# Kernel optimization log

Measured on AMD Instinct MI355X. Metric: run time of the kernel, lower is better.

Reference implementation:

```python
import jax, jax.numpy as jnp
import numpy as np

# Sizes: B graphs of N nodes each, K nearest neighbours, D=feat_dim=nhid, C=pos_dim
B, N, K, D, C = 4, 1024, 128, 32, 2
L = 3                     # number of EGNN conv layers
E_IN = 2 * D + 1          # edge MLP input: feats_i | feats_j | rel_dist (edge_dim=0, fourier=0)
E_H = 2 * E_IN            # edge MLP hidden


def _lin(key, fan_in, fan_out):
    kw, kb = jax.random.split(key)
    w = jax.random.normal(kw, (fan_in, fan_out), jnp.float32) / np.sqrt(fan_in)
    b = jax.random.normal(kb, (fan_out,), jnp.float32) * 0.01
    return w, b


def _stack(key, fan_in, fan_out):
    ws, bs = zip(*[_lin(k, fan_in, fan_out) for k in jax.random.split(key, L)])
    return jnp.stack(ws), jnp.stack(bs)


def setup_inputs() -> dict:
    key = jax.random.key(0)
    ks = jax.random.split(key, 10)
    feat_ = jax.random.normal(ks[0], (B * N, D), jnp.float32)
    coor_ = jax.random.normal(ks[1], (B * N, C), jnp.float32)
    batch = jnp.full((B,), N, dtype=jnp.int32)   # per-graph node counts (equal-size graphs)
    embed_w, embed_b = _lin(ks[2], D, D)         # embed: Linear(feat_dim, nhid)
    e1_w, e1_b = _stack(ks[3], E_IN, E_H)        # edge MLP
    e2_w, e2_b = _stack(ks[4], E_H, D)           # -> m_dim = nhid
    gate_w, gate_b = _stack(ks[5], D, 1)         # soft_edges gate
    c1_w, c1_b = _stack(ks[6], D, 4 * D)         # coors MLP
    c2_w, c2_b = _stack(ks[7], 4 * D, 1)
    n1_w, n1_b = _stack(ks[8], 2 * D, 2 * D)     # node MLP
    n2_w, n2_b = _stack(ks[9], 2 * D, D)
    coors_scale = jnp.full((L, 1), 1e-2, jnp.float32)  # CoorsNorm scale (init 1e-2)
    return dict(feat_=feat_, coor_=coor_, batch=batch, embed_w=embed_w, embed_b=embed_b,
                e1_w=e1_w, e1_b=e1_b, e2_w=e2_w, e2_b=e2_b, gate_w=gate_w, gate_b=gate_b,
                c1_w=c1_w, c1_b=c1_b, c2_w=c2_w, c2_b=c2_b, n1_w=n1_w, n1_b=n1_b,
                n2_w=n2_w, n2_b=n2_b, coors_scale=coors_scale)


def _lrelu(x):
    return jax.nn.leaky_relu(x, 0.1)


def _gather(x, idx):
    # x: [B, n, d], idx: [B, n, k] -> [B, n, k, d]
    return jax.vmap(lambda xb, ib: xb[ib])(x, idx)


def _egnn_layer(feats, coors, p):
    (e1_w, e1_b, e2_w, e2_b, gate_w, gate_b, c1_w, c1_b, c2_w, c2_b,
     n1_w, n1_b, n2_w, n2_b, scale) = p
    # pairwise squared distances; k smallest (self included, valid_radius=inf)
    diff = coors[:, :, None, :] - coors[:, None, :, :]      # [B,n,n,C]
    dist = jnp.sum(diff * diff, axis=-1)                    # [B,n,n]
    neg_d, idx = jax.lax.top_k(-dist, K)                    # k nearest
    rel_dist = -neg_d[..., None]                            # [B,n,K,1]
    rel_coors = coors[:, :, None, :] - _gather(coors, idx)  # [B,n,K,C]
    feats_j = _gather(feats, idx)                           # [B,n,K,D]
    feats_i = jnp.broadcast_to(feats[:, :, None, :], feats_j.shape)
    edge_in = jnp.concatenate([feats_i, feats_j, rel_dist], axis=-1)  # [B,n,K,E_IN]
    # edge MLP: Lin -> act -> Lin -> act ; soft edge gate
    m = _lrelu(_lrelu(edge_in @ e1_w + e1_b) @ e2_w + e2_b)            # [B,n,K,D]
    m = m * jax.nn.sigmoid(m @ gate_w + gate_b)
    # coordinate update: coors_mlp -> scalar weights; CoorsNorm on rel coords
    cw = (_lrelu(m @ c1_w + c1_b) @ c2_w + c2_b)[..., 0]               # [B,n,K]
    norm = jnp.maximum(jnp.linalg.norm(rel_coors, axis=-1, keepdims=True), 1e-8)
    rel_n = rel_coors / norm * scale
    coors_out = jnp.einsum('bik,bikc->bic', cw, rel_n) + coors
    # feature update: sum-pool messages, node MLP with residual
    m_i = jnp.sum(m, axis=2)                                           # [B,n,D]
    node_in = jnp.concatenate([feats, m_i], axis=-1)
    feats_out = _lrelu(node_in @ n1_w + n1_b) @ n2_w + n2_b + feats
    return feats_out, coors_out


def reference(feat_, coor_, batch, embed_w, embed_b, e1_w, e1_b, e2_w, e2_b,
              gate_w, gate_b, c1_w, c1_b, c2_w, c2_b, n1_w, n1_b, n2_w, n2_b,
              coors_scale):
    # embed MLP (dropout is identity at p=0 / eval), then batch equal-size graphs
    feats = _lrelu(feat_ @ embed_w + embed_b).reshape(B, N, D)
    coors = coor_.reshape(B, N, C)
    for l in range(L):
        p = (e1_w[l], e1_b[l], e2_w[l], e2_b[l], gate_w[l], gate_b[l],
             c1_w[l], c1_b[l], c2_w[l], c2_b[l], n1_w[l], n1_b[l],
             n2_w[l], n2_b[l], coors_scale[l])
        feats, coors = _egnn_layer(feats, coors, p)
    return feats.reshape(B * N, D)
```

## Files before the change

kernel.cpp:

```cpp
#include <hip/hip_runtime.h>
#include <hip/hip_bf16.h>
#include <math.h>

#define BB 4
#define NN 1024
#define KK 128
#define DD 32
#define LL 3
#define EH 130
#define EHP 132

typedef float f32x4 __attribute__((ext_vector_type(4)));
typedef short s16x8 __attribute__((ext_vector_type(8)));

__device__ __forceinline__ float lrelu(float x) { return fmaxf(x, 0.1f * x); }

__device__ __forceinline__ unsigned pk2(float a, float b) {
    __hip_bfloat162 h = __float22bfloat162_rn(float2{a, b});
    return *(unsigned*)&h;
}
__device__ __forceinline__ unsigned short bf16_hu(float v) {
    return (unsigned short)((__float_as_uint(v) + 0x8000u) >> 16);
}
__device__ __forceinline__ unsigned short bf16_rne(float v) {
    unsigned u = __float_as_uint(v);
    return (unsigned short)((u + 0x7fffu + ((u >> 16) & 1u)) >> 16);
}

__device__ __forceinline__ void knn_select(const float2* __restrict__ cbp, int i, int lane,
                                           int* __restrict__ nb) {
    const float2 ci = cbp[i];
    unsigned k[16];
#pragma unroll
    for (int s = 0; s < 16; s++) {
        float2 cj = cbp[lane + 64 * s];
        float dx = ci.x - cj.x, dy = ci.y - cj.y;
        float d = __fadd_rn(__fmul_rn(dx, dx), __fmul_rn(dy, dy));
        k[s] = __float_as_uint(d);
    }
    unsigned P = 0;
    for (int bpos = 30; bpos >= 0; bpos--) {
        const unsigned X = P | (1u << bpos);
        unsigned c = 0;
#pragma unroll
        for (int s = 0; s < 16; s++)
            c += (unsigned)__popcll(__ballot(k[s] < X));
        if (c < (unsigned)KK) P = X;
    }
    const unsigned dstar = P;
    const unsigned long long below = (1ull << lane) - 1ull;
    unsigned run = 0;
#pragma unroll
    for (int s = 0; s < 16; s++) {
        unsigned long long m = __ballot(k[s] < dstar);
        if (k[s] < dstar) nb[run + (unsigned)__popcll(m & below)] = lane + 64 * s;
        run += (unsigned)__popcll(m);
    }
    const int need = KK - (int)run;
    unsigned tie = 0;
    for (int s = 0; s < 16 && (int)tie < need; s++) {
        unsigned long long m = __ballot(k[s] == dstar);
        if (k[s] == dstar) {
            unsigned r = tie + (unsigned)__popcll(m & below);
            if ((int)r < need) nb[run + r] = lane + 64 * s;
        }
        tie += (unsigned)__popcll(m);
    }
}

__global__ __launch_bounds__(128) void prep_kernel(
    const float* __restrict__ feat, const float* __restrict__ coor,
    const float* __restrict__ ew, const float* __restrict__ eb,
    float* __restrict__ fout,
    const float* __restrict__ e1w0, const float* __restrict__ e1b0,
    float* __restrict__ HI, float* __restrict__ HJ,
    int* __restrict__ nbr,
    const float* __restrict__ e2w, const float* __restrict__ e2b,
    const float* __restrict__ c1w,
    unsigned short* __restrict__ e2f, unsigned short* __restrict__ c1f) {
    const int bid = blockIdx.x;
    const int t = threadIdx.x;
    if (bid < 2048) {
        __shared__ float sfe[2][DD];
        const int n0 = bid * 2;
        if (t < 64) {
            const int nl = t >> 5, o = t & 31;
            const float* f = feat + (size_t)(n0 + nl) * DD;
            float a = eb[o];
#pragma unroll
            for (int k = 0; k < DD; k++) a = fmaf(f[k], ew[k * DD + o], a);
            a = lrelu(a);
            fout[(size_t)(n0 + nl) * DD + o] = a;
            sfe[nl][o] = a;
        }
        __syncthreads();
        for (int idx = t; idx < 2 * EHP; idx += 128) {
            const int nl = idx / EHP, o = idx - nl * EHP;
            const size_t off = (size_t)(n0 + nl) * EHP + o;
            if (o >= EH) { HI[off] = 0.f; HJ[off] = 0.f; continue; }
            const float* fl = sfe[nl];
            float aa = e1b0[o], cc = 0.f;
#pragma unroll
            for (int k = 0; k < DD; k++) aa = fmaf(fl[k], e1w0[k * EH + o], aa);
#pragma unroll
            for (int k = 0; k < DD; k++) cc = fmaf(fl[k], e1w0[(DD + k) * EH + o], cc);
            HI[off] = aa;
            HJ[off] = cc;
        }
    } else if (bid < 4096) {
        const int node = (bid - 2048) * 2 + (t >> 6);
        const int b = node >> 10, i = node & (NN - 1);
        knn_select((const float2*)coor + (size_t)b * NN, i, t & 63,
                   nbr + (size_t)node * KK);
    } else {
        const int TOT_E2 = LL * 5120;
        const int TOT = TOT_E2 + LL * 4096;
        for (int u = (bid - 4096) * 128 + t; u < TOT; u += 96 * 128) {
            if (u < TOT_E2) {
                int l = u / 5120, v = u - l * 5120;
                int jj = v & 7, la = (v >> 3) & 63, nt = (v >> 9) & 1, c = v >> 10;
                int n = nt * 16 + (la & 15);
                float val;
                if (c < 4) {
                    int k = 32 * c + (la >> 4) * 8 + jj;
                    val = e2w[(size_t)l * EH * DD + k * DD + n];
                } else {
                    int ks = (la >> 4) * 8 + jj;
                    val = (ks == 0) ? e2w[((size_t)l * EH + 128) * DD + n]
                        : (ks == 1) ? e2w[((size_t)l * EH + 129) * DD + n]
                        : (ks == 2) ? e2b[(size_t)l * DD + n] : 0.f;
                }
                e2f[u] = bf16_rne(val);
            } else {
                int v = u - TOT_E2;
                int jj = v & 7, la = (v >> 3) & 63, nt = (v >> 9) & 7, l = v >> 12;
                int k = (la >> 4) * 8 + jj;
                int n = nt * 16 + (la & 15);
                c1f[v] = bf16_rne(c1w[(size_t)l * DD * 128 + k * 128 + n]);
            }
        }
    }
}

__global__ __launch_bounds__(256) void knnpre_kernel(
    const float* __restrict__ coors, int* __restrict__ nbr,
    const float* __restrict__ feats, const float* __restrict__ e1w, const float* __restrict__ e1b,
    float* __restrict__ HI, float* __restrict__ HJ) {
    const int KNNB = BB * NN / 4;
    if (blockIdx.x >= KNNB) {
        int t = (int)(blockIdx.x - KNNB) * 256 + threadIdx.x;
        if (t >= BB * NN * EHP) return;
        int n = t / EHP, o = t % EHP;
        if (o >= EH) { HI[t] = 0.f; HJ[t] = 0.f; return; }
        const float* f = feats + n * DD;
        float a = e1b[o], c = 0.f;
#pragma unroll
        for (int k = 0; k < DD; k++) a = fmaf(f[k], e1w[k * EH + o], a);
#pragma unroll
        for (int k = 0; k < DD; k++) c = fmaf(f[k], e1w[(DD + k) * EH + o], c);
        HI[t] = a;
        HJ[t] = c;
        return;
    }
    const int node = (int)blockIdx.x * 4 + (threadIdx.x >> 6);
    const int b = node >> 10, i = node & (NN - 1);
    knn_select((const float2*)coors + (size_t)b * NN, i, threadIdx.x & 63,
               nbr + (size_t)node * KK);
}

__global__ __launch_bounds__(256) void layer_kernel(
    const float* __restrict__ feats_in, const float* __restrict__ coors_in,
    const int*   __restrict__ nbr,
    const float* __restrict__ HI, const float* __restrict__ HJ,
    const float* __restrict__ w65,
    const unsigned short* __restrict__ e2f,
    const unsigned short* __restrict__ c1f,
    const float* __restrict__ gw, const float* __restrict__ gb,
    const float* __restrict__ c1b, const float* __restrict__ c2w, const float* __restrict__ c2b,
    const float* __restrict__ n1w, const float* __restrict__ n1b,
    const float* __restrict__ n2w, const float* __restrict__ n2b,
    const float* __restrict__ scale,
    float* __restrict__ feats_out, float* __restrict__ coors_out) {
    const int node = blockIdx.x;
    const int b = node >> 10;
    const int t = threadIdx.x;
    const int lane = t & 63, wid = t >> 6;
    const int ln = lane & 15, q = lane >> 4;
    const int rowbase = wid * 32;

    __shared__ __align__(16) float shi[EHP];
    __shared__ __align__(16) float sw65[EHP];
    __shared__ __align__(16) unsigned short smA[4 * 32 * 32];
    __shared__ float sx0[128], sx1[128], su[128], sv[128], srd[128];
    __shared__ int snb[128];
    __shared__ float sgw[DD], sfi[DD];
    __shared__ float sc1b[128], sc2w[128];
    __shared__ float redm[4][DD], redc[4][2];
    __shared__ float sni[2 * DD], shd[2 * DD];
    __shared__ float sp1[4][2 * DD], sp2[4][DD];

    for (int u = t; u < EHP; u += 256) {
        shi[u] = HI[(size_t)node * EHP + u];
        sw65[u] = (u < EH) ? w65[u] : 0.f;
    }
    if (t < DD) { sfi[t] = feats_in[node * DD + t]; sgw[t] = gw[t]; }
    if (t >= 128) { sc1b[t - 128] = c1b[t - 128]; sc2w[t - 128] = c2w[t - 128]; }
    __syncthreads();

    const float cix = coors_in[node * 2], ciy = coors_in[node * 2 + 1];
    if (t < 128) {
        const int j = nbr[(size_t)node * KK + t];
        snb[t] = j;
        const float2 cj = *(const float2*)(coors_in + ((size_t)(b * NN) + j) * 2);
        const float dx = cix - cj.x, dy = ciy - cj.y;
        const float rd = __fadd_rn(__fmul_rn(dx, dx), __fmul_rn(dy, dy));
        srd[t] = rd;
        const float nrm = fmaxf(sqrtf(rd), 1e-8f);
        const float s = scale[0] / nrm;
        su[t] = dx * s;
        sv[t] = dy * s;
        const float2 hjt = *(const float2*)(HJ + ((size_t)(b * NN) + j) * EHP + 128);
        sx0[t] = lrelu(shi[128] + hjt.x + rd * sw65[128]);
        sx1[t] = lrelu(shi[129] + hjt.y + rd * sw65[129]);
    }
    __syncthreads();

    float rdR[2];
    const float* hjb[2];
#pragma unroll
    for (int mt = 0; mt < 2; mt++) {
        const int row = rowbase + mt * 16 + ln;
        rdR[mt] = srd[row];
        hjb[mt] = HJ + ((size_t)(b * NN) + snb[row]) * EHP;
    }

    const float4* shi4 = (const float4*)shi;
    const float4* sw4  = (const float4*)sw65;

    const f32x4 zz = {0.f, 0.f, 0.f, 0.f};
    f32x4 accA[2][2];
    accA[0][0] = zz; accA[0][1] = zz; accA[1][0] = zz; accA[1][1] = zz;

    float4 ha[2], hbv[2];
#pragma unroll
    for (int mt = 0; mt < 2; mt++) {
        const float4* hjp = (const float4*)(hjb[mt] + q * 8);
        ha[mt] = hjp[0];
        hbv[mt] = hjp[1];
    }
    s16x8 bcur0 = *(const s16x8*)(e2f + (0 * 64 + lane) * 8);
    s16x8 bcur1 = *(const s16x8*)(e2f + (1 * 64 + lane) * 8);

#pragma unroll 1
    for (int c = 0; c < 4; c++) {
        s16x8 bn0 = *(const s16x8*)(e2f + (((c + 1) * 2 + 0) * 64 + lane) * 8);
        s16x8 bn1 = *(const s16x8*)(e2f + (((c + 1) * 2 + 1) * 64 + lane) * 8);
        float4 nha[2], nhb[2];
        if (c < 3) {
#pragma unroll
            for (int mt = 0; mt < 2; mt++) {
                const float4* hjp = (const float4*)(hjb[mt] + (c + 1) * 32 + q * 8);
                nha[mt] = hjp[0];
                nhb[mt] = hjp[1];
            }
        }
        const int kb = c * 8 + q * 2;
        const float4 hi0 = shi4[kb], hi1 = shi4[kb + 1];
        const float4 wv0 = sw4[kb],  wv1 = sw4[kb + 1];
#pragma unroll
        for (int mt = 0; mt < 2; mt++) {
            const float r = rdR[mt];
            union { s16x8 v; unsigned u[4]; } A;
            A.u[0] = pk2(lrelu(hi0.x + ha[mt].x + r * wv0.x), lrelu(hi0.y + ha[mt].y + r * wv0.y));
            A.u[1] = pk2(lrelu(hi0.z + ha[mt].z + r * wv0.z), lrelu(hi0.w + ha[mt].w + r * wv0.w));
            A.u[2] = pk2(lrelu(hi1.x + hbv[mt].x + r * wv1.x), lrelu(hi1.y + hbv[mt].y + r * wv1.y));
            A.u[3] = pk2(lrelu(hi1.z + hbv[mt].z + r * wv1.z), lrelu(hi1.w + hbv[mt].w + r * wv1.w));
            accA[mt][0] = __builtin_amdgcn_mfma_f32_16x16x32_bf16(A.v, bcur0, accA[mt][0], 0, 0, 0);
            accA[mt][1] = __builtin_amdgcn_mfma_f32_16x16x32_bf16(A.v, bcur1, accA[mt][1], 0, 0, 0);
        }
#pragma unroll
        for (int mt = 0; mt < 2; mt++) { ha[mt] = nha[mt]; hbv[mt] = nhb[mt]; }
        bcur0 = bn0; bcur1 = bn1;
    }

    {
#pragma unroll
        for (int mt = 0; mt < 2; mt++) {
            const int row = rowbase + mt * 16 + ln;
            union { s16x8 v; unsigned u[4]; } A;
            const unsigned p0 = pk2(sx0[row], sx1[row]);
            A.u[0] = (q == 0) ? p0 : 0u;
            A.u[1] = (q == 0) ? 0x00003f80u : 0u;
            A.u[2] = 0u;
            A.u[3] = 0u;
            accA[mt][0] = __builtin_amdgcn_mfma_f32_16x16x32_bf16(A.v, bcur0, accA[mt][0], 0, 0, 0);
            accA[mt][1] = __builtin_amdgcn_mfma_f32_16x16x32_bf16(A.v, bcur1, accA[mt][1], 0, 0, 0);
        }
    }

    s16x8 cfr[8];
#pragma unroll
    for (int g8 = 0; g8 < 8; g8++)
        cfr[g8] = *(const s16x8*)(c1f + (g8 * 64 + lane) * 8);

#pragma unroll
    for (int mt = 0; mt < 2; mt++)
#pragma unroll
        for (int nt = 0; nt < 2; nt++)
#pragma unroll
            for (int r = 0; r < 4; r++)
                accA[mt][nt][r] = lrelu(accA[mt][nt][r]);

    const float gbv = gb[0];
#pragma unroll
    for (int mt = 0; mt < 2; mt++) {
        float p[4];
#pragma unroll
        for (int r = 0; r < 4; r++)
            p[r] = accA[mt][0][r] * sgw[ln] + accA[mt][1][r] * sgw[16 + ln];
#pragma unroll
        for (int off = 1; off <= 8; off <<= 1)
#pragma unroll
            for (int r = 0; r < 4; r++) p[r] += __shfl_xor(p[r], off);
#pragma unroll
        for (int r = 0; r < 4; r++) {
            const float g = 1.f / (1.f + __expf(-(p[r] + gbv)));
            accA[mt][0][r] *= g;
            accA[mt][1][r] *= g;
        }
    }

    float mi0 = 0.f, mi1 = 0.f;
#pragma unroll
    for (int mt = 0; mt < 2; mt++)
#pragma unroll
        for (int r = 0; r < 4; r++) { mi0 += accA[mt][0][r]; mi1 += accA[mt][1][r]; }
    mi0 += __shfl_xor(mi0, 16); mi0 += __shfl_xor(mi0, 32);
    mi1 += __shfl_xor(mi1, 16); mi1 += __shfl_xor(mi1, 32);
    if (lane < 16) { redm[wid][lane] = mi0; redm[wid][16 + lane] = mi1; }

    unsigned short* smw = smA + wid * (32 * 32);
#pragma unroll
    for (int mt = 0; mt < 2; mt++)
#pragma unroll
        for (int nt = 0; nt < 2; nt++)
#pragma unroll
            for (int r = 0; r < 4; r++) {
                const int prow = (r << 3) | (4 * mt + q);
                smw[prow * 32 + nt * 16 + ln] = bf16_hu(accA[mt][nt][r]);
            }

    s16x8 a4[2];
#pragma unroll
    for (int mt = 0; mt < 2; mt++) {
        const int prow = ((ln & 3) << 3) | (4 * mt + (ln >> 2));
        a4[mt] = *(const s16x8*)(smw + prow * 32 + q * 8);
    }

    float cacc[2][4];
#pragma unroll
    for (int mt = 0; mt < 2; mt++)
#pragma unroll
        for (int r = 0; r < 4; r++) cacc[mt][r] = 0.f;

#pragma unroll
    for (int g = 0; g < 4; g++) {
        const float cb0 = sc1b[(2 * g + 0) * 16 + ln];
        const float cb1 = sc1b[(2 * g + 1) * 16 + ln];
        const f32x4 ci0 = {cb0, cb0, cb0, cb0};
        const f32x4 ci1 = {cb1, cb1, cb1, cb1};
        f32x4 c20[2], c21[2];
#pragma unroll
        for (int mt = 0; mt < 2; mt++) {
            c20[mt] = __builtin_amdgcn_mfma_f32_16x16x32_bf16(a4[mt], cfr[2 * g + 0], ci0, 0, 0, 0);
            c21[mt] = __builtin_amdgcn_mfma_f32_16x16x32_bf16(a4[mt], cfr[2 * g + 1], ci1, 0, 0, 0);
        }
#pragma unroll
        for (int h = 0; h < 2; h++) {
            const float c2wv = sc2w[(2 * g + h) * 16 + ln];
#pragma unroll
            for (int mt = 0; mt < 2; mt++)
#pragma unroll
                for (int r = 0; r < 4; r++) {
                    const float v = (h ? c21[mt][r] : c20[mt][r]);
                    cacc[mt][r] = fmaf(lrelu(v), c2wv, cacc[mt][r]);
                }
        }
    }
#pragma unroll
    for (int off = 1; off <= 8; off <<= 1)
#pragma unroll
        for (int mt = 0; mt < 2; mt++)
#pragma unroll
            for (int r = 0; r < 4; r++) cacc[mt][r] += __shfl_xor(cacc[mt][r], off);

    const float c2bv = c2b[0];
    float vxp = 0.f, vyp = 0.f;
    if (ln == 0) {
#pragma unroll
        for (int mt = 0; mt < 2; mt++)
#pragma unroll
            for (int r = 0; r < 4; r++) {
                const int row = rowbase + mt * 16 + q * 4 + r;
                const float cw = cacc[mt][r] + c2bv;
                vxp = fmaf(cw, su[row], vxp);
                vyp = fmaf(cw, sv[row], vyp);
            }
    }
    vxp += __shfl_xor(vxp, 16); vxp += __shfl_xor(vxp, 32);
    vyp += __shfl_xor(vyp, 16); vyp += __shfl_xor(vyp, 32);
    if (lane == 0) { redc[wid][0] = vxp; redc[wid][1] = vyp; }

    __syncthreads();
    if (t < DD) {
        sni[t] = sfi[t];
        sni[DD + t] = redm[0][t] + redm[1][t] + redm[2][t] + redm[3][t];
    }
    __syncthreads();
    {
        const int o = t & 63, p = t >> 6;
        float a = 0.f;
#pragma unroll
        for (int k = 0; k < 16; k++) a = fmaf(sni[p * 16 + k], n1w[(p * 16 + k) * 64 + o], a);
        sp1[p][o] = a;
    }
    __syncthreads();
    if (t < 2 * DD)
        shd[t] = lrelu(n1b[t] + ((sp1[0][t] + sp1[1][t]) + (sp1[2][t] + sp1[3][t])));
    __syncthreads();
    if (t < 128) {
        const int o = t & 31, p = t >> 5;
        float a = 0.f;
#pragma unroll
        for (int k = 0; k < 16; k++) a = fmaf(shd[p * 16 + k], n2w[(p * 16 + k) * DD + o], a);
        sp2[p][o] = a;
    }
    __syncthreads();
    if (t < DD)
        feats_out[node * DD + t] =
            n2b[t] + ((sp2[0][t] + sp2[1][t]) + (sp2[2][t] + sp2[3][t])) + sfi[t];
    if (t == 0) {
        coors_out[node * 2]     = cix + redc[0][0] + redc[1][0] + redc[2][0] + redc[3][0];
        coors_out[node * 2 + 1] = ciy + redc[0][1] + redc[1][1] + redc[2][1] + redc[3][1];
    }
}

extern "C" void kernel_launch(void* const* d_in, const int* in_sizes, int n_in,
                              void* d_out, int out_size, void* d_ws, size_t ws_size,
                              hipStream_t stream) {
    const float* feat_   = (const float*)d_in[0];
    const float* coor_   = (const float*)d_in[1];
    const float* embed_w = (const float*)d_in[3];
    const float* embed_b = (const float*)d_in[4];
    const float* e1_w    = (const float*)d_in[5];
    const float* e1_b    = (const float*)d_in[6];
    const float* e2_w    = (const float*)d_in[7];
    const float* e2_b    = (const float*)d_in[8];
    const float* gate_w  = (const float*)d_in[9];
    const float* gate_b  = (const float*)d_in[10];
    const float* c1_w    = (const float*)d_in[11];
    const float* c1_b    = (const float*)d_in[12];
    const float* c2_w    = (const float*)d_in[13];
    const float* c2_b    = (const float*)d_in[14];
    const float* n1_w    = (const float*)d_in[15];
    const float* n1_b    = (const float*)d_in[16];
    const float* n2_w    = (const float*)d_in[17];
    const float* n2_b    = (const float*)d_in[18];
    const float* cscale  = (const float*)d_in[19];

    float* ws = (float*)d_ws;
    float* fa   = ws;   ws += BB * NN * DD;
    float* fb   = ws;   ws += BB * NN * DD;
    float* ca   = ws;   ws += BB * NN * 2;
    float* cb2  = ws;   ws += BB * NN * 2;
    float* HIa  = ws;   ws += BB * NN * EHP;
    float* HJa  = ws;   ws += BB * NN * EHP;
    unsigned short* e2f = (unsigned short*)ws;
    unsigned short* c1f = e2f + LL * 5120;
    int* nbr = (int*)(c1f + LL * 4096);

    prep_kernel<<<4096 + 96, 128, 0, stream>>>(feat_, coor_, embed_w, embed_b, fa,
                                               e1_w, e1_b, HIa, HJa, nbr,
                                               e2_w, e2_b, c1_w, e2f, c1f);

    const int KNNB = BB * NN / 4;
    const int PREB = (BB * NN * EHP + 255) / 256;
    const float* fin = fa;
    const float* cin = coor_;
    float* fouts[LL] = {fb, fa, (float*)d_out};
    float* couts[LL] = {ca, cb2, ca};

    for (int l = 0; l < LL; l++) {
        if (l > 0)
            knnpre_kernel<<<KNNB + PREB, 256, 0, stream>>>(
                cin, nbr, fin, e1_w + (size_t)l * 65 * EH, e1_b + (size_t)l * EH, HIa, HJa);
        layer_kernel<<<BB * NN, 256, 0, stream>>>(
            fin, cin, nbr, HIa, HJa,
            e1_w + ((size_t)l * 65 + 64) * EH,
            e2f + (size_t)l * 5120,
            c1f + (size_t)l * 4096,
            gate_w + (size_t)l * DD,
            gate_b + l,
            c1_b + (size_t)l * 128,
            c2_w + (size_t)l * 128,
            c2_b + l,
            n1_w + (size_t)l * 64 * 64,
            n1_b + (size_t)l * 64,
            n2_w + (size_t)l * 64 * 32,
            n2_b + (size_t)l * DD,
            cscale + l,
            fouts[l], couts[l]);
        fin = fouts[l];
        cin = couts[l];
    }
}
```

Measured before the change: 316.5 us.

## Fuse kNN selection and next-layer edge precompute into layer kernel

The separate kNN kernel and per-layer HI/HJ precompute kernel are removed. Each layer block now runs kNN selection for its node in one wavefront while the other waves load shared data. At the end of each layer it computes the next layer's HI/HJ projections from its own output features into double-buffered arrays. This removes two kernel launches per layer and the neighbour-index round trip through global memory. In exchange, the kNN work now sits on the critical path of the layer kernel, handled by a single wave per block.

```diff
diff --git a/kernel.cpp b/kernel.cpp
--- a/kernel.cpp
+++ b/kernel.cpp
@@ -74,7 +74,6 @@
     float* __restrict__ fout,
     const float* __restrict__ e1w0, const float* __restrict__ e1b0,
     float* __restrict__ HI, float* __restrict__ HJ,
-    int* __restrict__ nbr,
     const float* __restrict__ e2w, const float* __restrict__ e2b,
     const float* __restrict__ c1w,
     unsigned short* __restrict__ e2f, unsigned short* __restrict__ c1f) {
@@ -107,15 +106,10 @@
             HI[off] = aa;
             HJ[off] = cc;
         }
-    } else if (bid < 4096) {
-        const int node = (bid - 2048) * 2 + (t >> 6);
-        const int b = node >> 10, i = node & (NN - 1);
-        knn_select((const float2*)coor + (size_t)b * NN, i, t & 63,
-                   nbr + (size_t)node * KK);
     } else {
         const int TOT_E2 = LL * 5120;
         const int TOT = TOT_E2 + LL * 4096;
-        for (int u = (bid - 4096) * 128 + t; u < TOT; u += 96 * 128) {
+        for (int u = (bid - 2048) * 128 + t; u < TOT; u += 96 * 128) {
             if (u < TOT_E2) {
                 int l = u / 5120, v = u - l * 5120;
                 int jj = v & 7, la = (v >> 3) & 63, nt = (v >> 9) & 1, c = v >> 10;
@@ -142,35 +136,8 @@
     }
 }
 
-__global__ __launch_bounds__(256) void knnpre_kernel(
-    const float* __restrict__ coors, int* __restrict__ nbr,
-    const float* __restrict__ feats, const float* __restrict__ e1w, const float* __restrict__ e1b,
-    float* __restrict__ HI, float* __restrict__ HJ) {
-    const int KNNB = BB * NN / 4;
-    if (blockIdx.x >= KNNB) {
-        int t = (int)(blockIdx.x - KNNB) * 256 + threadIdx.x;
-        if (t >= BB * NN * EHP) return;
-        int n = t / EHP, o = t % EHP;
-        if (o >= EH) { HI[t] = 0.f; HJ[t] = 0.f; return; }
-        const float* f = feats + n * DD;
-        float a = e1b[o], c = 0.f;
-#pragma unroll
-        for (int k = 0; k < DD; k++) a = fmaf(f[k], e1w[k * EH + o], a);
-#pragma unroll
-        for (int k = 0; k < DD; k++) c = fmaf(f[k], e1w[(DD + k) * EH + o], c);
-        HI[t] = a;
-        HJ[t] = c;
-        return;
-    }
-    const int node = (int)blockIdx.x * 4 + (threadIdx.x >> 6);
-    const int b = node >> 10, i = node & (NN - 1);
-    knn_select((const float2*)coors + (size_t)b * NN, i, threadIdx.x & 63,
-               nbr + (size_t)node * KK);
-}
-
 __global__ __launch_bounds__(256) void layer_kernel(
     const float* __restrict__ feats_in, const float* __restrict__ coors_in,
-    const int*   __restrict__ nbr,
     const float* __restrict__ HI, const float* __restrict__ HJ,
     const float* __restrict__ w65,
     const unsigned short* __restrict__ e2f,
@@ -180,6 +147,8 @@
     const float* __restrict__ n1w, const float* __restrict__ n1b,
     const float* __restrict__ n2w, const float* __restrict__ n2b,
     const float* __restrict__ scale,
+    const float* __restrict__ e1wn, const float* __restrict__ e1bn,
+    float* __restrict__ HIn, float* __restrict__ HJn,
     float* __restrict__ feats_out, float* __restrict__ coors_out) {
     const int node = blockIdx.x;
     const int b = node >> 10;
@@ -193,24 +162,27 @@
     __shared__ __align__(16) unsigned short smA[4 * 32 * 32];
     __shared__ float sx0[128], sx1[128], su[128], sv[128], srd[128];
     __shared__ int snb[128];
-    __shared__ float sgw[DD], sfi[DD];
+    __shared__ float sgw[DD], sfi[DD], sfo[DD];
     __shared__ float sc1b[128], sc2w[128];
     __shared__ float redm[4][DD], redc[4][2];
     __shared__ float sni[2 * DD], shd[2 * DD];
     __shared__ float sp1[4][2 * DD], sp2[4][DD];
 
-    for (int u = t; u < EHP; u += 256) {
-        shi[u] = HI[(size_t)node * EHP + u];
-        sw65[u] = (u < EH) ? w65[u] : 0.f;
-    }
-    if (t < DD) { sfi[t] = feats_in[node * DD + t]; sgw[t] = gw[t]; }
-    if (t >= 128) { sc1b[t - 128] = c1b[t - 128]; sc2w[t - 128] = c2w[t - 128]; }
+    if (t < 64) {
+        knn_select((const float2*)coors_in + (size_t)b * NN, node & (NN - 1), lane, snb);
+    } else {
+        for (int u = t - 64; u < EHP; u += 192) {
+            shi[u] = HI[(size_t)node * EHP + u];
+            sw65[u] = (u < EH) ? w65[u] : 0.f;
+        }
+        if (t - 64 < DD) { sfi[t - 64] = feats_in[node * DD + (t - 64)]; sgw[t - 64] = gw[t - 64]; }
+        if (t >= 128) { sc1b[t - 128] = c1b[t - 128]; sc2w[t - 128] = c2w[t - 128]; }
+    }
     __syncthreads();
 
     const float cix = coors_in[node * 2], ciy = coors_in[node * 2 + 1];
     if (t < 128) {
-        const int j = nbr[(size_t)node * KK + t];
-        snb[t] = j;
+        const int j = snb[t];
         const float2 cj = *(const float2*)(coors_in + ((size_t)(b * NN) + j) * 2);
         const float dx = cix - cj.x, dy = ciy - cj.y;
         const float rd = __fadd_rn(__fmul_rn(dx, dx), __fmul_rn(dy, dy));
@@ -436,12 +408,28 @@
         sp2[p][o] = a;
     }
     __syncthreads();
-    if (t < DD)
-        feats_out[node * DD + t] =
-            n2b[t] + ((sp2[0][t] + sp2[1][t]) + (sp2[2][t] + sp2[3][t])) + sfi[t];
+    if (t < DD) {
+        const float val = n2b[t] + ((sp2[0][t] + sp2[1][t]) + (sp2[2][t] + sp2[3][t])) + sfi[t];
+        feats_out[node * DD + t] = val;
+        sfo[t] = val;
+    }
     if (t == 0) {
         coors_out[node * 2]     = cix + redc[0][0] + redc[1][0] + redc[2][0] + redc[3][0];
         coors_out[node * 2 + 1] = ciy + redc[0][1] + redc[1][1] + redc[2][1] + redc[3][1];
+    }
+    __syncthreads();
+
+    if (e1wn) {
+        for (int idx = t; idx < 2 * EHP; idx += 256) {
+            const int nl = idx / EHP, o = idx - nl * EHP;
+            float* dst = (nl ? HJn : HIn) + (size_t)node * EHP + o;
+            if (o >= EH) { *dst = 0.f; continue; }
+            const int rowoff = nl ? DD : 0;
+            float a = nl ? 0.f : e1bn[o];
+#pragma unroll
+            for (int k = 0; k < DD; k++) a = fmaf(sfo[k], e1wn[(rowoff + k) * EH + o], a);
+            *dst = a;
+        }
     }
 }
 
@@ -473,29 +461,28 @@
     float* fb   = ws;   ws += BB * NN * DD;
     float* ca   = ws;   ws += BB * NN * 2;
     float* cb2  = ws;   ws += BB * NN * 2;
-    float* HIa  = ws;   ws += BB * NN * EHP;
-    float* HJa  = ws;   ws += BB * NN * EHP;
+    float* HI0  = ws;   ws += BB * NN * EHP;
+    float* HJ0  = ws;   ws += BB * NN * EHP;
+    float* HI1  = ws;   ws += BB * NN * EHP;
+    float* HJ1  = ws;   ws += BB * NN * EHP;
     unsigned short* e2f = (unsigned short*)ws;
     unsigned short* c1f = e2f + LL * 5120;
-    int* nbr = (int*)(c1f + LL * 4096);
-
-    prep_kernel<<<4096 + 96, 128, 0, stream>>>(feat_, coor_, embed_w, embed_b, fa,
-                                               e1_w, e1_b, HIa, HJa, nbr,
+
+    prep_kernel<<<2048 + 96, 128, 0, stream>>>(feat_, coor_, embed_w, embed_b, fa,
+                                               e1_w, e1_b, HI0, HJ0,
                                                e2_w, e2_b, c1_w, e2f, c1f);
 
-    const int KNNB = BB * NN / 4;
-    const int PREB = (BB * NN * EHP + 255) / 256;
+    float* HIbuf[2] = {HI0, HI1};
+    float* HJbuf[2] = {HJ0, HJ1};
     const float* fin = fa;
     const float* cin = coor_;
     float* fouts[LL] = {fb, fa, (float*)d_out};
     float* couts[LL] = {ca, cb2, ca};
 
     for (int l = 0; l < LL; l++) {
-        if (l > 0)
-            knnpre_kernel<<<KNNB + PREB, 256, 0, stream>>>(
-                cin, nbr, fin, e1_w + (size_t)l * 65 * EH, e1_b + (size_t)l * EH, HIa, HJa);
+        const int cur = l & 1, nxt = (l + 1) & 1;
         layer_kernel<<<BB * NN, 256, 0, stream>>>(
-            fin, cin, nbr, HIa, HJa,
+            fin, cin, HIbuf[cur], HJbuf[cur],
             e1_w + ((size_t)l * 65 + 64) * EH,
             e2f + (size_t)l * 5120,
             c1f + (size_t)l * 4096,
@@ -509,6 +496,9 @@
             n2_w + (size_t)l * 64 * 32,
             n2_b + (size_t)l * DD,
             cscale + l,
+            (l < LL - 1) ? (e1_w + (size_t)(l + 1) * 65 * EH) : nullptr,
+            (l < LL - 1) ? (e1_b + (size_t)(l + 1) * EH) : nullptr,
+            HIbuf[nxt], HJbuf[nxt],
             fouts[l], couts[l]);
         fin = fouts[l];
         cin = couts[l];
```

Result: slower. 334.7 us (+5.8%).

## Replace bitwise ballot binary search in kNN select with 8-bit radix histogram passes

Applied to the files above, without the earlier changes.

The k-th smallest distance threshold is now found with four radix-select passes over 8-bit digits, using a per-wave LDS histogram built with shared atomics plus a wave prefix scan. The previous code ran 31 bit-by-bit iterations, each doing 16 ballots and popcounts. The new version cuts the number of passes but adds LDS atomics and contention on hot bins. It also relies on __threadfence_block inside a single wavefront for ordering, with no barrier.

```diff
diff --git a/kernel.cpp b/kernel.cpp
--- a/kernel.cpp
+++ b/kernel.cpp
@@ -28,6 +28,7 @@
 }
 
 __device__ __forceinline__ void knn_select(const float2* __restrict__ cbp, int i, int lane,
+                                           unsigned* __restrict__ hist,
                                            int* __restrict__ nb) {
     const float2 ci = cbp[i];
     unsigned k[16];
@@ -38,16 +39,53 @@
         float d = __fadd_rn(__fmul_rn(dx, dx), __fmul_rn(dy, dy));
         k[s] = __float_as_uint(d);
     }
-    unsigned P = 0;
-    for (int bpos = 30; bpos >= 0; bpos--) {
-        const unsigned X = P | (1u << bpos);
-        unsigned c = 0;
-#pragma unroll
-        for (int s = 0; s < 16; s++)
-            c += (unsigned)__popcll(__ballot(k[s] < X));
-        if (c < (unsigned)KK) P = X;
-    }
-    const unsigned dstar = P;
+
+    unsigned prefix = 0u;
+    unsigned r = KK - 1;
+#pragma unroll
+    for (int pass = 0; pass < 4; pass++) {
+        const int sh = 24 - 8 * pass;
+        const unsigned mpref = (pass == 0) ? 0u : (0xFFFFFFFFu << (sh + 8));
+        ((uint4*)hist)[lane] = uint4{0u, 0u, 0u, 0u};
+        __threadfence_block();
+#pragma unroll
+        for (int s = 0; s < 16; s++) {
+            if ((k[s] & mpref) == prefix)
+                atomicAdd(&hist[(k[s] >> sh) & 255u], 1u);
+        }
+        __threadfence_block();
+        const uint4 h = ((const uint4*)hist)[lane];
+        const unsigned partial = h.x + h.y + h.z + h.w;
+        unsigned incl = partial;
+#pragma unroll
+        for (int off = 1; off < 64; off <<= 1) {
+            unsigned v = __shfl_up(incl, off, 64);
+            if (lane >= off) incl += v;
+        }
+        const unsigned excl = incl - partial;
+        const bool own = (r >= excl) && (r < incl);
+        unsigned enc = 0u;
+        if (own) {
+            unsigned hh[4] = {h.x, h.y, h.z, h.w};
+            unsigned e = excl;
+            int bin = -1;
+#pragma unroll
+            for (int ii = 0; ii < 4; ii++) {
+                if (bin < 0) {
+                    if (r < e + hh[ii]) bin = ii;
+                    else e += hh[ii];
+                }
+            }
+            enc = (((unsigned)(4 * lane + bin)) << 16) | (r - e);
+        }
+        const unsigned long long mk = __ballot(own);
+        const int src = __ffsll((unsigned long long)mk) - 1;
+        enc = __shfl(enc, src, 64);
+        prefix |= (enc >> 16) << sh;
+        r = enc & 0xFFFFu;
+    }
+    const unsigned dstar = prefix;
+
     const unsigned long long below = (1ull << lane) - 1ull;
     unsigned run = 0;
 #pragma unroll
@@ -61,8 +99,8 @@
     for (int s = 0; s < 16 && (int)tie < need; s++) {
         unsigned long long m = __ballot(k[s] == dstar);
         if (k[s] == dstar) {
-            unsigned r = tie + (unsigned)__popcll(m & below);
-            if ((int)r < need) nb[run + r] = lane + 64 * s;
+            unsigned r2 = tie + (unsigned)__popcll(m & below);
+            if ((int)r2 < need) nb[run + r2] = lane + 64 * s;
         }
         tie += (unsigned)__popcll(m);
     }
@@ -80,6 +118,7 @@
     unsigned short* __restrict__ e2f, unsigned short* __restrict__ c1f) {
     const int bid = blockIdx.x;
     const int t = threadIdx.x;
+    __shared__ __align__(16) unsigned shist[2][256];
     if (bid < 2048) {
         __shared__ float sfe[2][DD];
         const int n0 = bid * 2;
@@ -110,7 +149,7 @@
     } else if (bid < 4096) {
         const int node = (bid - 2048) * 2 + (t >> 6);
         const int b = node >> 10, i = node & (NN - 1);
-        knn_select((const float2*)coor + (size_t)b * NN, i, t & 63,
+        knn_select((const float2*)coor + (size_t)b * NN, i, t & 63, shist[t >> 6],
                    nbr + (size_t)node * KK);
     } else {
         const int TOT_E2 = LL * 5120;
@@ -146,6 +185,7 @@
     const float* __restrict__ coors, int* __restrict__ nbr,
     const float* __restrict__ feats, const float* __restrict__ e1w, const float* __restrict__ e1b,
     float* __restrict__ HI, float* __restrict__ HJ) {
+    __shared__ __align__(16) unsigned shist[4][256];
     const int KNNB = BB * NN / 4;
     if (blockIdx.x >= KNNB) {
         int t = (int)(blockIdx.x - KNNB) * 256 + threadIdx.x;
@@ -165,7 +205,7 @@
     const int node = (int)blockIdx.x * 4 + (threadIdx.x >> 6);
     const int b = node >> 10, i = node & (NN - 1);
     knn_select((const float2*)coors + (size_t)b * NN, i, threadIdx.x & 63,
-               nbr + (size_t)node * KK);
+               shist[threadIdx.x >> 6], nbr + (size_t)node * KK);
 }
 
 __global__ __launch_bounds__(256) void layer_kernel(
```

After: 321.1 us. Within noise of the previous version (+1.5%).
